# Kernel tuning notes

Hardware: AMD Instinct MI355X
Metric: run time of the kernel (lower is better)

Reference implementation:

```python
import jax, jax.numpy as jnp
import numpy as np

KSIZE = 5  # smoothing_kernel_size


def _gauss_kernel(size):
    n = size // 2
    sigma = n / 3.0
    k = np.exp(-np.arange(-n, n + 1, dtype=np.float32) ** 2 / (2.0 * sigma ** 2))
    k = k / k.sum()
    return jnp.asarray(k[:, None] * k[None, :])  # (size, size)


def _prob_map(pts, H, W, kernel):
    """pts: (B,N,2) yx subpixel keypoints -> (B,N,H*W) L2-normalized prob maps."""
    B, N = pts.shape[:2]
    fl = jnp.floor(pts)
    ce = jnp.ceil(pts)
    # 4 neighbors: (fy,fx),(fy,cx),(cy,fx),(cy,cx) -- matches nidx fancy-index in torch
    ny = jnp.stack([fl[..., 0], fl[..., 0], ce[..., 0], ce[..., 0]], -1)  # (B,N,4)
    nx = jnp.stack([fl[..., 1], ce[..., 1], fl[..., 1], ce[..., 1]], -1)
    nb = jnp.stack([ny, nx], -1)  # (B,N,4,2)
    # torch.pairwise_distance adds eps=1e-6 to the difference
    d = jnp.sqrt(jnp.sum((nb - pts[:, :, None, :] + 1e-6) ** 2, -1))  # (B,N,4)
    t = d / jnp.maximum(jnp.sum(d, -1, keepdims=True), 1e-12)  # L1 normalize
    lin = ny.astype(jnp.int32) * W + nx.astype(jnp.int32)  # (B,N,4) flat bin idx
    bi = jnp.arange(B)[:, None, None]
    ni = jnp.arange(N)[None, :, None]
    prob = jnp.zeros((B, N, H * W), pts.dtype).at[bi, ni, lin].add(t)
    prob = prob.reshape(B * N, 1, H, W)
    if kernel is not None:
        prob = jax.lax.conv_general_dilated(prob, kernel[None, None], (1, 1), 'SAME')
    prob = prob.reshape(B, N, H * W)
    nrm = jnp.sqrt(jnp.sum(prob ** 2, -1, keepdims=True))
    return prob / jnp.maximum(nrm, 1e-12)  # L2 normalize (torch eps=1e-12)


def _interp_rows(vol, pts):
    """Bilinear gather. vol: (B,H,W,C); pts: (B,N,2) yx. Returns (B,N,C).
    Equivalent to grid_sample(align_corners=True) at in-bounds pixel coords."""
    H, W = vol.shape[1], vol.shape[2]
    y, x = pts[..., 0], pts[..., 1]
    y0f = jnp.floor(y)
    x0f = jnp.floor(x)
    wy = (y - y0f)[..., None]
    wx = (x - x0f)[..., None]
    y0 = jnp.clip(y0f.astype(jnp.int32), 0, H - 1)
    x0 = jnp.clip(x0f.astype(jnp.int32), 0, W - 1)
    y1 = jnp.clip(y0 + 1, 0, H - 1)
    x1 = jnp.clip(x0 + 1, 0, W - 1)
    b = jnp.arange(vol.shape[0])[:, None]
    v00 = vol[b, y0, x0]
    v01 = vol[b, y0, x1]
    v10 = vol[b, y1, x0]
    v11 = vol[b, y1, x1]
    return ((1 - wy) * (1 - wx)) * v00 + ((1 - wy) * wx) * v01 + \
           (wy * (1 - wx)) * v10 + (wy * wx) * v11


def setup_inputs() -> dict:
    key = jax.random.key(0)
    k1, k2 = jax.random.split(key)
    B, H, W, N = 8, 64, 64, 128
    corr = jax.random.normal(k1, (B, H, W, H, W), jnp.float32)
    # keypoints in [0, H-1) so floor/ceil bins and bilinear gather stay in-bounds
    kp = jax.random.uniform(k2, (B, N, 2, 2), jnp.float32) * (H - 1 - 1e-3)
    return {"corr": corr, "kp": kp}


def reference(corr, kp):
    B, H, W = corr.shape[0], corr.shape[1], corr.shape[2]
    kernel = _gauss_kernel(KSIZE)
    pts1 = kp[..., 0]
    pts2 = kp[..., 1]
    # direction img1 -> img2: spatial (H1,W1), channels = flattened (H2,W2)
    target12 = _prob_map(pts2, H, W, kernel)
    pred12 = _interp_rows(corr.reshape(B, H, W, H * W), pts1)
    loss1 = jnp.mean(jnp.sqrt(jnp.sum((pred12 - target12) ** 2, axis=(-1, -2))))
    # direction img2 -> img1: spatial (H2,W2), channels = flattened (H1,W1)
    target21 = _prob_map(pts1, H, W, kernel)
    vol21 = jnp.transpose(corr, (0, 3, 4, 1, 2)).reshape(B, H, W, H * W)
    pred21 = _interp_rows(vol21, pts2)
    loss2 = jnp.mean(jnp.sqrt(jnp.sum((pred21 - target21) ** 2, axis=(-1, -2))))
    return loss1 + loss2
```

## Files before the change

### kernel.cpp

```cpp
#include <hip/hip_runtime.h>
#include <math.h>

#define BB 8
#define HH 64
#define WW 64
#define NN 128
#define CC (HH*WW)

__device__ __forceinline__ float sqf(float x){ return x*x; }


__global__ void lpml_zero(float* __restrict__ acc21)
{
  const int i = threadIdx.x + blockIdx.x * 256;
  if (i < BB*NN) acc21[i] = 0.f;
}

__global__ __launch_bounds__(256) void lpml_stream21(
    const float* __restrict__ corr, const float* __restrict__ kp,
    float* __restrict__ acc21)
{
  const int bidx = blockIdx.x;
  const int half = bidx & 1;
  const int y1   = (bidx >> 1) & (HH-1);
  const int b    = bidx >> 7;
  const int tid  = threadIdx.x;

  __shared__ float plane[2][CC];
  __shared__ int   soff[NN][4];
  __shared__ float swt[NN][4];
  __shared__ float red[256];

  if (tid < NN) {
    const float* kpp = kp + (size_t)(b*NN + tid)*4;
    const float sy = kpp[1], sx = kpp[3];
    const float y0f = floorf(sy), x0f = floorf(sx);
    const float wy = sy - y0f, wx = sx - x0f;
    int Y0 = (int)y0f; Y0 = Y0 < 0 ? 0 : (Y0 > HH-1 ? HH-1 : Y0);
    int X0 = (int)x0f; X0 = X0 < 0 ? 0 : (X0 > WW-1 ? WW-1 : X0);
    const int Y1 = (Y0+1 > HH-1) ? HH-1 : Y0+1;
    const int X1 = (X0+1 > WW-1) ? WW-1 : X0+1;
    soff[tid][0] = Y0*WW + X0; soff[tid][1] = Y0*WW + X1;
    soff[tid][2] = Y1*WW + X0; soff[tid][3] = Y1*WW + X1;
    swt[tid][0] = (1.f-wy)*(1.f-wx); swt[tid][1] = (1.f-wy)*wx;
    swt[tid][2] = wy*(1.f-wx);       swt[tid][3] = wy*wx;
  }
  __syncthreads();

  const int n = tid & (NN-1);
  const int g = tid >> 7;
  const int o00 = soff[n][0], o01 = soff[n][1], o10 = soff[n][2], o11 = soff[n][3];
  const float w00 = swt[n][0], w01 = swt[n][1], w10 = swt[n][2], w11 = swt[n][3];

  const size_t rowbase = (((size_t)b*HH + y1)*WW + (size_t)half*32) * CC;
  float accv = 0.f;
  for (int it = 0; it < 16; ++it) {
    const float4* src = (const float4*)(corr + rowbase + (size_t)(2*it)*CC);
    float4* dst = (float4*)(&plane[0][0]);
#pragma unroll
    for (int k = 0; k < 8; ++k) dst[tid + 256*k] = src[tid + 256*k];
    __syncthreads();
    const float* P = &plane[g][0];
    const float v = w00*P[o00] + w01*P[o01] + w10*P[o10] + w11*P[o11];
    accv += v*v;
    __syncthreads();
  }

  red[tid] = accv; __syncthreads();
  if (tid < NN) atomicAdd(&acc21[b*NN + n], red[tid] + red[tid+NN]);
}

__global__ __launch_bounds__(256) void lpml_main(
    const float* __restrict__ corr, const float* __restrict__ kp,
    float* __restrict__ partial)
{
  const int tid  = threadIdx.x;
  const int bidx = blockIdx.x;
  const int dir  = bidx >> 10;
  const int b    = (bidx >> 7) & 7;
  const int n    = bidx & 127;

  __shared__ float red[256];

  const float* kpp = kp + (size_t)(b*NN + n)*4;
  const float p1y = kpp[0], p2y = kpp[1], p1x = kpp[2], p2x = kpp[3];

  const float sy = dir ? p2y : p1y;
  const float sx = dir ? p2x : p1x;
  const float ty = dir ? p1y : p2y;
  const float tx = dir ? p1x : p2x;

  const float y0f = floorf(sy), x0f = floorf(sx);
  const float wy = sy - y0f, wx = sx - x0f;
  int Y0 = (int)y0f; Y0 = Y0 < 0 ? 0 : (Y0 > HH-1 ? HH-1 : Y0);
  int X0 = (int)x0f; X0 = X0 < 0 ? 0 : (X0 > WW-1 ? WW-1 : X0);
  const int Y1 = (Y0+1 > HH-1) ? HH-1 : Y0+1;
  const int X1 = (X0+1 > WW-1) ? WW-1 : X0+1;
  const float w00 = (1.f-wy)*(1.f-wx), w01 = (1.f-wy)*wx;
  const float w10 = wy*(1.f-wx),       w11 = wy*wx;

  const size_t bbase = (size_t)b * HH * WW * CC;

  const float* r00 = corr + bbase + (size_t)(Y0*WW + X0) * CC;
  const float* r01 = corr + bbase + (size_t)(Y0*WW + X1) * CC;
  const float* r10 = corr + bbase + (size_t)(Y1*WW + X0) * CC;
  const float* r11 = corr + bbase + (size_t)(Y1*WW + X1) * CC;
  const int o00 = Y0*WW + X0, o01 = Y0*WW + X1;
  const int o10 = Y1*WW + X0, o11 = Y1*WW + X1;

  float ss = 0.f;
  if (dir == 0) {
    for (int c0 = tid*4; c0 < CC; c0 += 1024) {
      const float4 a  = *(const float4*)(r00 + c0);
      const float4 bq = *(const float4*)(r01 + c0);
      const float4 cq = *(const float4*)(r10 + c0);
      const float4 dq = *(const float4*)(r11 + c0);
      const float p0 = w00*a.x + w01*bq.x + w10*cq.x + w11*dq.x;
      const float p1 = w00*a.y + w01*bq.y + w10*cq.y + w11*dq.y;
      const float p2 = w00*a.z + w01*bq.z + w10*cq.z + w11*dq.z;
      const float p3 = w00*a.w + w01*bq.w + w10*cq.w + w11*dq.w;
      ss += p0*p0 + p1*p1 + p2*p2 + p3*p3;
    }
  }
  red[tid] = ss; __syncthreads();
  for (int s = 128; s > 0; s >>= 1) { if (tid < s) red[tid] += red[tid+s]; __syncthreads(); }
  const float S = red[0]; __syncthreads();

  float k1d[5];
  {
    float ksum = 0.f;
#pragma unroll
    for (int i = 0; i < 5; ++i) { const float d = (float)(i-2); k1d[i] = expf(-d*d*1.125f); ksum += k1d[i]; }
#pragma unroll
    for (int i = 0; i < 5; ++i) k1d[i] /= ksum;
  }

  const float fy = floorf(ty), cy = ceilf(ty);
  const float fx = floorf(tx), cx = ceilf(tx);
  const float d0 = sqrtf(sqf(fy-ty+1e-6f) + sqf(fx-tx+1e-6f));
  const float d1 = sqrtf(sqf(fy-ty+1e-6f) + sqf(cx-tx+1e-6f));
  const float d2 = sqrtf(sqf(cy-ty+1e-6f) + sqf(fx-tx+1e-6f));
  const float d3 = sqrtf(sqf(cy-ty+1e-6f) + sqf(cx-tx+1e-6f));
  const float sd = fmaxf(d0+d1+d2+d3, 1e-12f);
  const float t0 = d0/sd, t1 = d1/sd, t2 = d2/sd, t3 = d3/sd;
  const int ify = (int)fy, ifx = (int)fx;
  const int ddy = (int)cy - ify, ddx = (int)cx - ifx;
  const float loc00 = t0 + (ddx==0?t1:0.f) + (ddy==0?t2:0.f) + ((ddy==0&&ddx==0)?t3:0.f);
  const float loc01 = (ddx==1?t1:0.f) + ((ddy==0&&ddx==1)?t3:0.f);
  const float loc10 = (ddy==1?t2:0.f) + ((ddy==1&&ddx==0)?t3:0.f);
  const float loc11 = ((ddy==1&&ddx==1)?t3:0.f);

  float val = 0.f;
  int by = 0, bx = 0;
  bool inb = false;
  if (tid < 36) {
    const int r = tid / 6, c = tid % 6;
    by = ify - 2 + r; bx = ifx - 2 + c;
    inb = (by >= 0 && by < HH && bx >= 0 && bx < WW);
    if (inb) {
      const float kr0 = (r <= 4) ? k1d[r]   : 0.f;
      const float kr1 = (r >= 1) ? k1d[r-1] : 0.f;
      const float kc0 = (c <= 4) ? k1d[c]   : 0.f;
      const float kc1 = (c >= 1) ? k1d[c-1] : 0.f;
      val = loc00*kr0*kc0 + loc01*kr0*kc1 + loc10*kr1*kc0 + loc11*kr1*kc1;
    }
  }

  red[tid] = inb ? val*val : 0.f; __syncthreads();
  for (int s = 128; s > 0; s >>= 1) { if (tid < s) red[tid] += red[tid+s]; __syncthreads(); }
  const float nrm2 = red[0]; __syncthreads();
  const float nrmc = fmaxf(sqrtf(nrm2), 1e-12f);
  const float tgtsq = nrm2 / (nrmc*nrmc);

  float dc = 0.f;
  if (tid < 36 && inb) {
    float predbin;
    if (dir == 0) {
      const int cbin = by*WW + bx;
      predbin = w00*r00[cbin] + w01*r01[cbin] + w10*r10[cbin] + w11*r11[cbin];
    } else {
      const float* slab = corr + bbase + (size_t)(by*WW + bx) * CC;
      predbin = w00*slab[o00] + w01*slab[o01] + w10*slab[o10] + w11*slab[o11];
    }
    dc = (val / nrmc) * predbin;
  }
  red[tid] = dc; __syncthreads();
  for (int s = 128; s > 0; s >>= 1) { if (tid < s) red[tid] += red[tid+s]; __syncthreads(); }

  if (tid == 0) partial[bidx] = S - 2.f*red[0] + tgtsq;
}

__global__ void lpml_reduce(const float* __restrict__ partial,
                            const float* __restrict__ acc21,
                            float* __restrict__ out)
{
  __shared__ float sh[16];
  const int tid = threadIdx.x;
  if (tid < 16) {
    const int dir = tid >> 3, b = tid & 7;
    const float* p = partial + dir*(BB*NN) + b*NN;
    float s = 0.f;
    if (dir == 0) { for (int i = 0; i < NN; ++i) s += p[i]; }
    else          { for (int i = 0; i < NN; ++i) s += p[i] + acc21[b*NN + i]; }
    sh[tid] = sqrtf(s);
  }
  __syncthreads();
  if (tid == 0) {
    float l1 = 0.f, l2 = 0.f;
    for (int i = 0; i < BB; ++i) { l1 += sh[i]; l2 += sh[8+i]; }
    out[0] = l1/(float)BB + l2/(float)BB;
  }
}

extern "C" void kernel_launch(void* const* d_in, const int* in_sizes, int n_in,
                              void* d_out, int out_size, void* d_ws, size_t ws_size,
                              hipStream_t stream) {
  const float* corr = (const float*)d_in[0];
  const float* kp   = (const float*)d_in[1];
  float* partial = (float*)d_ws;
  float* acc21   = (float*)d_ws + 2*BB*NN;

  hipLaunchKernelGGL(lpml_zero, dim3((BB*NN + 255)/256), dim3(256), 0, stream, acc21);
  hipLaunchKernelGGL(lpml_stream21, dim3(BB*HH*2), dim3(256), 0, stream,
                     corr, kp, acc21);
  hipLaunchKernelGGL(lpml_main, dim3(2*BB*NN), dim3(256), 0, stream,
                     corr, kp, partial);
  hipLaunchKernelGGL(lpml_reduce, dim3(1), dim3(64), 0, stream,
                     partial, acc21, (float*)d_out);
}
```

Baseline: 117.2 us.

## Fuse streaming and per-keypoint kernels into one interleaved launch

The separate streaming kernel for the img2→img1 squared-norm term and the per-keypoint main kernel are merged into one launch. Even blocks stream corr planes and odd blocks handle both directions for one keypoint, replacing the old half-idle dir=1 blocks. Per-keypoint partials now go straight to per-batch sums with atomics, and the target reductions use wave shuffles instead of shared-memory trees. This removes a launch and lets the bandwidth-heavy streaming work overlap the gather work. In exchange, every block reserves the large shared-memory plane, which may limit occupancy for the gather blocks, and float atomic ordering becomes nondeterministic.

Result: slower. 135.8 us (+15.9%).

```diff
diff --git a/kernel.cpp b/kernel.cpp
--- a/kernel.cpp
+++ b/kernel.cpp
@@ -9,132 +9,21 @@
 
 __device__ __forceinline__ float sqf(float x){ return x*x; }
 
-
-__global__ void lpml_zero(float* __restrict__ acc21)
+__device__ __forceinline__ float wsum64(float v){
+#pragma unroll
+  for (int k = 1; k < 64; k <<= 1) v += __shfl_xor(v, k, 64);
+  return v;
+}
+
+
+__global__ void lpml_zero(float* __restrict__ sums){
+  if (threadIdx.x < 16) sums[threadIdx.x] = 0.f;
+}
+
+__device__ __forceinline__ void target_bin(
+    float ty, float tx, const float* k1d, int lane,
+    float& val, int& by, int& bx, bool& inb)
 {
-  const int i = threadIdx.x + blockIdx.x * 256;
-  if (i < BB*NN) acc21[i] = 0.f;
-}
-
-__global__ __launch_bounds__(256) void lpml_stream21(
-    const float* __restrict__ corr, const float* __restrict__ kp,
-    float* __restrict__ acc21)
-{
-  const int bidx = blockIdx.x;
-  const int half = bidx & 1;
-  const int y1   = (bidx >> 1) & (HH-1);
-  const int b    = bidx >> 7;
-  const int tid  = threadIdx.x;
-
-  __shared__ float plane[2][CC];
-  __shared__ int   soff[NN][4];
-  __shared__ float swt[NN][4];
-  __shared__ float red[256];
-
-  if (tid < NN) {
-    const float* kpp = kp + (size_t)(b*NN + tid)*4;
-    const float sy = kpp[1], sx = kpp[3];
-    const float y0f = floorf(sy), x0f = floorf(sx);
-    const float wy = sy - y0f, wx = sx - x0f;
-    int Y0 = (int)y0f; Y0 = Y0 < 0 ? 0 : (Y0 > HH-1 ? HH-1 : Y0);
-    int X0 = (int)x0f; X0 = X0 < 0 ? 0 : (X0 > WW-1 ? WW-1 : X0);
-    const int Y1 = (Y0+1 > HH-1) ? HH-1 : Y0+1;
-    const int X1 = (X0+1 > WW-1) ? WW-1 : X0+1;
-    soff[tid][0] = Y0*WW + X0; soff[tid][1] = Y0*WW + X1;
-    soff[tid][2] = Y1*WW + X0; soff[tid][3] = Y1*WW + X1;
-    swt[tid][0] = (1.f-wy)*(1.f-wx); swt[tid][1] = (1.f-wy)*wx;
-    swt[tid][2] = wy*(1.f-wx);       swt[tid][3] = wy*wx;
-  }
-  __syncthreads();
-
-  const int n = tid & (NN-1);
-  const int g = tid >> 7;
-  const int o00 = soff[n][0], o01 = soff[n][1], o10 = soff[n][2], o11 = soff[n][3];
-  const float w00 = swt[n][0], w01 = swt[n][1], w10 = swt[n][2], w11 = swt[n][3];
-
-  const size_t rowbase = (((size_t)b*HH + y1)*WW + (size_t)half*32) * CC;
-  float accv = 0.f;
-  for (int it = 0; it < 16; ++it) {
-    const float4* src = (const float4*)(corr + rowbase + (size_t)(2*it)*CC);
-    float4* dst = (float4*)(&plane[0][0]);
-#pragma unroll
-    for (int k = 0; k < 8; ++k) dst[tid + 256*k] = src[tid + 256*k];
-    __syncthreads();
-    const float* P = &plane[g][0];
-    const float v = w00*P[o00] + w01*P[o01] + w10*P[o10] + w11*P[o11];
-    accv += v*v;
-    __syncthreads();
-  }
-
-  red[tid] = accv; __syncthreads();
-  if (tid < NN) atomicAdd(&acc21[b*NN + n], red[tid] + red[tid+NN]);
-}
-
-__global__ __launch_bounds__(256) void lpml_main(
-    const float* __restrict__ corr, const float* __restrict__ kp,
-    float* __restrict__ partial)
-{
-  const int tid  = threadIdx.x;
-  const int bidx = blockIdx.x;
-  const int dir  = bidx >> 10;
-  const int b    = (bidx >> 7) & 7;
-  const int n    = bidx & 127;
-
-  __shared__ float red[256];
-
-  const float* kpp = kp + (size_t)(b*NN + n)*4;
-  const float p1y = kpp[0], p2y = kpp[1], p1x = kpp[2], p2x = kpp[3];
-
-  const float sy = dir ? p2y : p1y;
-  const float sx = dir ? p2x : p1x;
-  const float ty = dir ? p1y : p2y;
-  const float tx = dir ? p1x : p2x;
-
-  const float y0f = floorf(sy), x0f = floorf(sx);
-  const float wy = sy - y0f, wx = sx - x0f;
-  int Y0 = (int)y0f; Y0 = Y0 < 0 ? 0 : (Y0 > HH-1 ? HH-1 : Y0);
-  int X0 = (int)x0f; X0 = X0 < 0 ? 0 : (X0 > WW-1 ? WW-1 : X0);
-  const int Y1 = (Y0+1 > HH-1) ? HH-1 : Y0+1;
-  const int X1 = (X0+1 > WW-1) ? WW-1 : X0+1;
-  const float w00 = (1.f-wy)*(1.f-wx), w01 = (1.f-wy)*wx;
-  const float w10 = wy*(1.f-wx),       w11 = wy*wx;
-
-  const size_t bbase = (size_t)b * HH * WW * CC;
-
-  const float* r00 = corr + bbase + (size_t)(Y0*WW + X0) * CC;
-  const float* r01 = corr + bbase + (size_t)(Y0*WW + X1) * CC;
-  const float* r10 = corr + bbase + (size_t)(Y1*WW + X0) * CC;
-  const float* r11 = corr + bbase + (size_t)(Y1*WW + X1) * CC;
-  const int o00 = Y0*WW + X0, o01 = Y0*WW + X1;
-  const int o10 = Y1*WW + X0, o11 = Y1*WW + X1;
-
-  float ss = 0.f;
-  if (dir == 0) {
-    for (int c0 = tid*4; c0 < CC; c0 += 1024) {
-      const float4 a  = *(const float4*)(r00 + c0);
-      const float4 bq = *(const float4*)(r01 + c0);
-      const float4 cq = *(const float4*)(r10 + c0);
-      const float4 dq = *(const float4*)(r11 + c0);
-      const float p0 = w00*a.x + w01*bq.x + w10*cq.x + w11*dq.x;
-      const float p1 = w00*a.y + w01*bq.y + w10*cq.y + w11*dq.y;
-      const float p2 = w00*a.z + w01*bq.z + w10*cq.z + w11*dq.z;
-      const float p3 = w00*a.w + w01*bq.w + w10*cq.w + w11*dq.w;
-      ss += p0*p0 + p1*p1 + p2*p2 + p3*p3;
-    }
-  }
-  red[tid] = ss; __syncthreads();
-  for (int s = 128; s > 0; s >>= 1) { if (tid < s) red[tid] += red[tid+s]; __syncthreads(); }
-  const float S = red[0]; __syncthreads();
-
-  float k1d[5];
-  {
-    float ksum = 0.f;
-#pragma unroll
-    for (int i = 0; i < 5; ++i) { const float d = (float)(i-2); k1d[i] = expf(-d*d*1.125f); ksum += k1d[i]; }
-#pragma unroll
-    for (int i = 0; i < 5; ++i) k1d[i] /= ksum;
-  }
-
   const float fy = floorf(ty), cy = ceilf(ty);
   const float fx = floorf(tx), cx = ceilf(tx);
   const float d0 = sqrtf(sqf(fy-ty+1e-6f) + sqf(fx-tx+1e-6f));
@@ -150,11 +39,9 @@
   const float loc10 = (ddy==1?t2:0.f) + ((ddy==1&&ddx==0)?t3:0.f);
   const float loc11 = ((ddy==1&&ddx==1)?t3:0.f);
 
-  float val = 0.f;
-  int by = 0, bx = 0;
-  bool inb = false;
-  if (tid < 36) {
-    const int r = tid / 6, c = tid % 6;
+  val = 0.f; by = 0; bx = 0; inb = false;
+  if (lane < 36) {
+    const int r = lane / 6, c = lane % 6;
     by = ify - 2 + r; bx = ifx - 2 + c;
     inb = (by >= 0 && by < HH && bx >= 0 && bx < WW);
     if (inb) {
@@ -165,50 +52,170 @@
       val = loc00*kr0*kc0 + loc01*kr0*kc1 + loc10*kr1*kc0 + loc11*kr1*kc1;
     }
   }
-
-  red[tid] = inb ? val*val : 0.f; __syncthreads();
-  for (int s = 128; s > 0; s >>= 1) { if (tid < s) red[tid] += red[tid+s]; __syncthreads(); }
-  const float nrm2 = red[0]; __syncthreads();
-  const float nrmc = fmaxf(sqrtf(nrm2), 1e-12f);
-  const float tgtsq = nrm2 / (nrmc*nrmc);
-
-  float dc = 0.f;
-  if (tid < 36 && inb) {
-    float predbin;
-    if (dir == 0) {
-      const int cbin = by*WW + bx;
-      predbin = w00*r00[cbin] + w01*r01[cbin] + w10*r10[cbin] + w11*r11[cbin];
-    } else {
-      const float* slab = corr + bbase + (size_t)(by*WW + bx) * CC;
-      predbin = w00*slab[o00] + w01*slab[o01] + w10*slab[o10] + w11*slab[o11];
-    }
-    dc = (val / nrmc) * predbin;
+}
+
+__global__ __launch_bounds__(256) void lpml_fused(
+    const float* __restrict__ corr, const float* __restrict__ kp,
+    float* __restrict__ sums)
+{
+  const int tid = threadIdx.x;
+  const bool is_stream = (blockIdx.x & 1) == 0;
+  const int idx = blockIdx.x >> 1;
+  const int b = idx >> 7;
+  const size_t bbase = (size_t)b * CC * CC;
+
+  __shared__ float plane[2][CC];
+  __shared__ int   soff[NN][4];
+  __shared__ float swt[NN][4];
+  __shared__ float red[256];
+
+  if (is_stream) {
+    const int half = idx & 1;
+    const int y1   = (idx >> 1) & (HH-1);
+
+    if (tid < NN) {
+      const float* kpp = kp + (size_t)(b*NN + tid)*4;
+      const float sy = kpp[1], sx = kpp[3];
+      const float y0f = floorf(sy), x0f = floorf(sx);
+      const float wy = sy - y0f, wx = sx - x0f;
+      int Y0 = (int)y0f; Y0 = Y0 < 0 ? 0 : (Y0 > HH-1 ? HH-1 : Y0);
+      int X0 = (int)x0f; X0 = X0 < 0 ? 0 : (X0 > WW-1 ? WW-1 : X0);
+      const int Y1 = (Y0+1 > HH-1) ? HH-1 : Y0+1;
+      const int X1 = (X0+1 > WW-1) ? WW-1 : X0+1;
+      soff[tid][0] = Y0*WW + X0; soff[tid][1] = Y0*WW + X1;
+      soff[tid][2] = Y1*WW + X0; soff[tid][3] = Y1*WW + X1;
+      swt[tid][0] = (1.f-wy)*(1.f-wx); swt[tid][1] = (1.f-wy)*wx;
+      swt[tid][2] = wy*(1.f-wx);       swt[tid][3] = wy*wx;
+    }
+    __syncthreads();
+
+    const int n = tid & (NN-1);
+    const int g = tid >> 7;
+    const int o00 = soff[n][0], o01 = soff[n][1], o10 = soff[n][2], o11 = soff[n][3];
+    const float w00 = swt[n][0], w01 = swt[n][1], w10 = swt[n][2], w11 = swt[n][3];
+
+    const size_t rowbase = (((size_t)b*HH + y1)*WW + (size_t)half*32) * CC;
+    float accv = 0.f;
+    for (int it = 0; it < 16; ++it) {
+      const float4* src = (const float4*)(corr + rowbase + (size_t)(2*it)*CC);
+      float4* dst = (float4*)(&plane[0][0]);
+#pragma unroll
+      for (int k = 0; k < 8; ++k) dst[tid + 256*k] = src[tid + 256*k];
+      __syncthreads();
+      const float* P = &plane[g][0];
+      const float v = w00*P[o00] + w01*P[o01] + w10*P[o10] + w11*P[o11];
+      accv += v*v;
+      __syncthreads();
+    }
+
+    red[tid] = accv; __syncthreads();
+    for (int s = 128; s > 0; s >>= 1) { if (tid < s) red[tid] += red[tid+s]; __syncthreads(); }
+    if (tid == 0) atomicAdd(&sums[8 + b], red[0]);
+
+  } else {
+    const int n = idx & 127;
+    const float* kpp = kp + (size_t)(b*NN + n)*4;
+    const float p1y = kpp[0], p2y = kpp[1], p1x = kpp[2], p2x = kpp[3];
+
+    const float y0fa = floorf(p1y), x0fa = floorf(p1x);
+    const float wya = p1y - y0fa, wxa = p1x - x0fa;
+    int Y0a = (int)y0fa; Y0a = Y0a < 0 ? 0 : (Y0a > HH-1 ? HH-1 : Y0a);
+    int X0a = (int)x0fa; X0a = X0a < 0 ? 0 : (X0a > WW-1 ? WW-1 : X0a);
+    const int Y1a = (Y0a+1 > HH-1) ? HH-1 : Y0a+1;
+    const int X1a = (X0a+1 > WW-1) ? WW-1 : X0a+1;
+    const float w00a = (1.f-wya)*(1.f-wxa), w01a = (1.f-wya)*wxa;
+    const float w10a = wya*(1.f-wxa),       w11a = wya*wxa;
+    const float* r00 = corr + bbase + (size_t)(Y0a*WW + X0a) * CC;
+    const float* r01 = corr + bbase + (size_t)(Y0a*WW + X1a) * CC;
+    const float* r10 = corr + bbase + (size_t)(Y1a*WW + X0a) * CC;
+    const float* r11 = corr + bbase + (size_t)(Y1a*WW + X1a) * CC;
+
+    const float y0fb = floorf(p2y), x0fb = floorf(p2x);
+    const float wyb = p2y - y0fb, wxb = p2x - x0fb;
+    int Y0b = (int)y0fb; Y0b = Y0b < 0 ? 0 : (Y0b > HH-1 ? HH-1 : Y0b);
+    int X0b = (int)x0fb; X0b = X0b < 0 ? 0 : (X0b > WW-1 ? WW-1 : X0b);
+    const int Y1b = (Y0b+1 > HH-1) ? HH-1 : Y0b+1;
+    const int X1b = (X0b+1 > WW-1) ? WW-1 : X0b+1;
+    const float w00b = (1.f-wyb)*(1.f-wxb), w01b = (1.f-wyb)*wxb;
+    const float w10b = wyb*(1.f-wxb),       w11b = wyb*wxb;
+    const int o00b = Y0b*WW + X0b, o01b = Y0b*WW + X1b;
+    const int o10b = Y1b*WW + X0b, o11b = Y1b*WW + X1b;
+
+    float ss = 0.f;
+    for (int c0 = tid*4; c0 < CC; c0 += 1024) {
+      const float4 a  = *(const float4*)(r00 + c0);
+      const float4 bq = *(const float4*)(r01 + c0);
+      const float4 cq = *(const float4*)(r10 + c0);
+      const float4 dq = *(const float4*)(r11 + c0);
+      const float p0 = w00a*a.x + w01a*bq.x + w10a*cq.x + w11a*dq.x;
+      const float p1 = w00a*a.y + w01a*bq.y + w10a*cq.y + w11a*dq.y;
+      const float p2 = w00a*a.z + w01a*bq.z + w10a*cq.z + w11a*dq.z;
+      const float p3 = w00a*a.w + w01a*bq.w + w10a*cq.w + w11a*dq.w;
+      ss += p0*p0 + p1*p1 + p2*p2 + p3*p3;
+    }
+    red[tid] = ss; __syncthreads();
+    for (int s = 128; s > 0; s >>= 1) { if (tid < s) red[tid] += red[tid+s]; __syncthreads(); }
+    const float S0 = red[0];
+
+    if (tid < 64) {
+      float k1d[5];
+      {
+        float ksum = 0.f;
+#pragma unroll
+        for (int i = 0; i < 5; ++i) { const float d = (float)(i-2); k1d[i] = expf(-d*d*1.125f); ksum += k1d[i]; }
+#pragma unroll
+        for (int i = 0; i < 5; ++i) k1d[i] /= ksum;
+      }
+
+      float tot0;
+      {
+        float val; int by, bx; bool inb;
+        target_bin(p2y, p2x, k1d, tid, val, by, bx, inb);
+        const float nrm2 = wsum64(inb ? val*val : 0.f);
+        const float nrmc = fmaxf(sqrtf(nrm2), 1e-12f);
+        const float T = nrm2 / (nrmc*nrmc);
+        float dc = 0.f;
+        if (inb) {
+          const int cbin = by*WW + bx;
+          const float predbin = w00a*r00[cbin] + w01a*r01[cbin]
+                              + w10a*r10[cbin] + w11a*r11[cbin];
+          dc = (val / nrmc) * predbin;
+        }
+        const float D = wsum64(dc);
+        tot0 = S0 - 2.f*D + T;
+      }
+      float tot1;
+      {
+        float val; int by, bx; bool inb;
+        target_bin(p1y, p1x, k1d, tid, val, by, bx, inb);
+        const float nrm2 = wsum64(inb ? val*val : 0.f);
+        const float nrmc = fmaxf(sqrtf(nrm2), 1e-12f);
+        const float T = nrm2 / (nrmc*nrmc);
+        float dc = 0.f;
+        if (inb) {
+          const float* slab = corr + bbase + (size_t)(by*WW + bx) * CC;
+          const float predbin = w00b*slab[o00b] + w01b*slab[o01b]
+                              + w10b*slab[o10b] + w11b*slab[o11b];
+          dc = (val / nrmc) * predbin;
+        }
+        const float D = wsum64(dc);
+        tot1 = -2.f*D + T;
+      }
+      if (tid == 0) {
+        atomicAdd(&sums[b],     tot0);
+        atomicAdd(&sums[8 + b], tot1);
+      }
+    }
   }
-  red[tid] = dc; __syncthreads();
-  for (int s = 128; s > 0; s >>= 1) { if (tid < s) red[tid] += red[tid+s]; __syncthreads(); }
-
-  if (tid == 0) partial[bidx] = S - 2.f*red[0] + tgtsq;
-}
-
-__global__ void lpml_reduce(const float* __restrict__ partial,
-                            const float* __restrict__ acc21,
-                            float* __restrict__ out)
+}
+
+__global__ void lpml_reduce(const float* __restrict__ sums, float* __restrict__ out)
 {
-  __shared__ float sh[16];
-  const int tid = threadIdx.x;
-  if (tid < 16) {
-    const int dir = tid >> 3, b = tid & 7;
-    const float* p = partial + dir*(BB*NN) + b*NN;
-    float s = 0.f;
-    if (dir == 0) { for (int i = 0; i < NN; ++i) s += p[i]; }
-    else          { for (int i = 0; i < NN; ++i) s += p[i] + acc21[b*NN + i]; }
-    sh[tid] = sqrtf(s);
-  }
-  __syncthreads();
-  if (tid == 0) {
-    float l1 = 0.f, l2 = 0.f;
-    for (int i = 0; i < BB; ++i) { l1 += sh[i]; l2 += sh[8+i]; }
-    out[0] = l1/(float)BB + l2/(float)BB;
+  if (threadIdx.x == 0) {
+    float l = 0.f;
+#pragma unroll
+    for (int b = 0; b < BB; ++b) l += sqrtf(sums[b]) + sqrtf(sums[8 + b]);
+    out[0] = l / (float)BB;
   }
 }
 
@@ -217,14 +224,9 @@
                               hipStream_t stream) {
   const float* corr = (const float*)d_in[0];
   const float* kp   = (const float*)d_in[1];
-  float* partial = (float*)d_ws;
-  float* acc21   = (float*)d_ws + 2*BB*NN;
-
-  hipLaunchKernelGGL(lpml_zero, dim3((BB*NN + 255)/256), dim3(256), 0, stream, acc21);
-  hipLaunchKernelGGL(lpml_stream21, dim3(BB*HH*2), dim3(256), 0, stream,
-                     corr, kp, acc21);
-  hipLaunchKernelGGL(lpml_main, dim3(2*BB*NN), dim3(256), 0, stream,
-                     corr, kp, partial);
-  hipLaunchKernelGGL(lpml_reduce, dim3(1), dim3(64), 0, stream,
-                     partial, acc21, (float*)d_out);
-}
+  float* sums = (float*)d_ws;
+
+  hipLaunchKernelGGL(lpml_zero,  dim3(1),    dim3(64),  0, stream, sums);
+  hipLaunchKernelGGL(lpml_fused, dim3(2048), dim3(256), 0, stream, corr, kp, sums);
+  hipLaunchKernelGGL(lpml_reduce, dim3(1),   dim3(64),  0, stream, sums, (float*)d_out);
+}
```
